# Kernel tuning notes

Hardware: AMD Instinct MI355X
Metric: run time of the kernel (lower is better)

## Reference

```python
import jax, jax.numpy as jnp
import numpy as np

N = 65536   # total nodes
E = 1048576 # total edges (avg degree 16)
B = 512     # graphs in batch
H = 4       # gat1 heads
C = 64      # per-head channels / GNN_HIDDEN


def segment_softmax(logits, seg, num_segments):
    # numerically stable softmax over segments (PyG softmax semantics, eps=1e-16)
    m = jax.ops.segment_max(logits, seg, num_segments=num_segments)
    m = jnp.where(jnp.isfinite(m), m, 0.0)
    e = jnp.exp(logits - m[seg])
    s = jax.ops.segment_sum(e, seg, num_segments=num_segments)
    return e / (s[seg] + 1e-16)


def gat_conv(x, edge_index, edge_attr, W, att_src, att_dst, We, att_edge, bias, heads, out_ch, concat):
    # PyG GATConv with edge_dim, add_self_loops=False
    n = x.shape[0]
    h = (x @ W).reshape(n, heads, out_ch)                 # (N,H,C)
    src, dst = edge_index[0], edge_index[1]
    a_s = jnp.sum(h * att_src, axis=-1)                   # (N,H)
    a_d = jnp.sum(h * att_dst, axis=-1)                   # (N,H)
    he = (edge_attr @ We).reshape(-1, heads, out_ch)      # (E,H,C)
    a_e = jnp.sum(he * att_edge, axis=-1)                 # (E,H)
    alpha = jax.nn.leaky_relu(a_s[src] + a_d[dst] + a_e, negative_slope=0.2)
    alpha = segment_softmax(alpha, dst, n)                # softmax over incoming edges per dst
    out = jax.ops.segment_sum(h[src] * alpha[..., None], dst, num_segments=n)  # (N,H,C)
    out = out.reshape(n, heads * out_ch) if concat else out.mean(axis=1)
    return out + bias


def setup_inputs() -> dict:
    key = jax.random.key(0)
    ks = jax.random.split(key, 24)
    s = 0.05
    d = {}
    d["global_feat"] = jax.random.normal(ks[0], (B, 512), jnp.float32)
    d["x"] = jax.random.normal(ks[1], (N, 13), jnp.float32)
    d["roi_feats"] = jax.random.normal(ks[2], (N, 256), jnp.float32)
    d["edge_index"] = jax.random.randint(ks[3], (2, E), 0, N)
    d["edge_attr"] = jax.random.normal(ks[4], (E, 5), jnp.float32)
    d["batch_vec"] = jnp.sort(jax.random.randint(ks[5], (N,), 0, B))
    # roi_proj / scene_proj
    d["roi_W"] = jax.random.normal(ks[6], (256, 64), jnp.float32) * s
    d["roi_b"] = jnp.zeros((64,), jnp.float32)
    d["scene_W"] = jax.random.normal(ks[7], (512, 128), jnp.float32) * s
    d["scene_b"] = jnp.zeros((128,), jnp.float32)
    d["g1_W"] = jax.random.normal(ks[8], (77, H * C), jnp.float32) * s
    d["g1_att_src"] = jax.random.normal(ks[9], (H, C), jnp.float32) * s
    d["g1_att_dst"] = jax.random.normal(ks[10], (H, C), jnp.float32) * s
    d["g1_We"] = jax.random.normal(ks[11], (5, H * C), jnp.float32) * s
    d["g1_att_edge"] = jax.random.normal(ks[12], (H, C), jnp.float32) * s
    d["g1_bias"] = jnp.zeros((H * C,), jnp.float32)
    # gat2: 256 -> 64, 1 head
    d["g2_W"] = jax.random.normal(ks[13], (H * C, C), jnp.float32) * s
    d["g2_att_src"] = jax.random.normal(ks[14], (1, C), jnp.float32) * s
    d["g2_att_dst"] = jax.random.normal(ks[15], (1, C), jnp.float32) * s
    d["g2_We"] = jax.random.normal(ks[16], (5, C), jnp.float32) * s
    d["g2_att_edge"] = jax.random.normal(ks[17], (1, C), jnp.float32) * s
    d["g2_bias"] = jnp.zeros((C,), jnp.float32)
    # attention pooling gate + classifier
    d["gate_W"] = jax.random.normal(ks[18], (C, 1), jnp.float32) * s
    d["gate_b"] = jnp.zeros((1,), jnp.float32)
    d["cls1_W"] = jax.random.normal(ks[19], (128 + C, 64), jnp.float32) * s
    d["cls1_b"] = jnp.zeros((64,), jnp.float32)
    d["cls2_W"] = jax.random.normal(ks[20], (64, 3), jnp.float32) * s
    d["cls2_b"] = jnp.zeros((3,), jnp.float32)
    return d


def reference(global_feat, x, roi_feats, edge_index, edge_attr, batch_vec,
              roi_W, roi_b, scene_W, scene_b,
              g1_W, g1_att_src, g1_att_dst, g1_We, g1_att_edge, g1_bias,
              g2_W, g2_att_src, g2_att_dst, g2_We, g2_att_edge, g2_bias,
              gate_W, gate_b, cls1_W, cls1_b, cls2_W, cls2_b):
    scene = global_feat @ scene_W + scene_b                       # (B,128)
    vis = jax.nn.relu(roi_feats @ roi_W + roi_b)                  # (N,64)
    h = jnp.concatenate([x, vis], axis=-1)                        # (N,77)
    h = jax.nn.relu(gat_conv(h, edge_index, edge_attr, g1_W, g1_att_src, g1_att_dst, g1_We, g1_att_edge, g1_bias, H, C, True))
    h = gat_conv(h, edge_index, edge_attr, g2_W, g2_att_src, g2_att_dst, g2_We, g2_att_edge, g2_bias, 1, C, False)  # (N,64)
    # GlobalAttention pooling
    gate = segment_softmax((h @ gate_W + gate_b)[:, 0], batch_vec, B)
    rel = jax.ops.segment_sum(gate[:, None] * h, batch_vec, num_segments=B)  # (B,64)
    comb = jnp.concatenate([scene, rel], axis=-1)                 # (B,192)
    hid = jax.nn.relu(comb @ cls1_W + cls1_b)                     # dropout off (eval)
    return hid @ cls2_W + cls2_b                                  # (B,3)
```

## Files before the change

kernel.cpp:

```cpp
#include <hip/hip_runtime.h>

#define N_NODES 65536
#define N_EDGES 1048576
#define NB      512

typedef unsigned short u16;
typedef unsigned int   u32;
typedef unsigned long long u64;

typedef __attribute__((ext_vector_type(8))) short bf16x8;
typedef __attribute__((ext_vector_type(4))) float f32x4;

__device__ __forceinline__ float bf2f(u16 u) { return __uint_as_float(((u32)u) << 16); }
__device__ __forceinline__ float lo16(u32 u) { return __uint_as_float(u << 16); }
__device__ __forceinline__ float hi16(u32 u) { return __uint_as_float(u & 0xffff0000u); }
__device__ __forceinline__ u16 f2bf(float f) {
    u32 u = __float_as_uint(f);
    u32 r = (u + 0x7fffu + ((u >> 16) & 1u)) >> 16;
    return (u16)r;
}
__device__ __forceinline__ u32 pk2(float a, float b) {
    return (u32)f2bf(a) | ((u32)f2bf(b) << 16);
}
__device__ __forceinline__ float wsum(float v) {
    for (int o = 32; o; o >>= 1) v += __shfl_xor(v, o, 64);
    return v;
}
__device__ __forceinline__ float wmax(float v) {
    for (int o = 32; o; o >>= 1) v = fmaxf(v, __shfl_xor(v, o, 64));
    return v;
}

__global__ void k_prep(const float* g1We, const float* g1ae, const float* g2We, const float* g2ae,
                       float* M1, float* M2) {
    int t = threadIdx.x;
    if (t < 20) {
        int j = t >> 2, h = t & 3;
        float s = 0.f;
        for (int c = 0; c < 64; c++) s += g1We[j * 256 + h * 64 + c] * g1ae[h * 64 + c];
        M1[t] = s;
    } else if (t < 25) {
        int j = t - 20;
        float s = 0.f;
        for (int c = 0; c < 64; c++) s += g2We[j * 64 + c] * g2ae[c];
        M2[j] = s;
    }
}

__global__ void k_wt1(const float* __restrict__ g1W, u16* __restrict__ Wt) {
    int c = blockIdx.x;
    int k = threadIdx.x;
    float v = 0.f;
    if (k < 77) {
        int ko = (k < 64) ? (13 + k) : (k - 64);
        v = g1W[(size_t)ko * 256 + c];
    }
    Wt[(size_t)c * 128 + k] = f2bf(v);
}

__global__ void k_prepv(const u16* __restrict__ Wt, const float* __restrict__ as_,
                        const float* __restrict__ ad_, float* __restrict__ v1s,
                        float* __restrict__ v1d) {
    int t = threadIdx.x;
    int h = t >> 7, k = t & 127;
    float s = 0.f, d = 0.f;
    for (int cc = 0; cc < 64; cc++) {
        float wv_ = bf2f(Wt[(size_t)(h * 64 + cc) * 128 + k]);
        s += wv_ * as_[h * 64 + cc];
        d += wv_ * ad_[h * 64 + cc];
    }
    v1s[t] = s;
    v1d[t] = d;
}

__global__ void k_wtv(const float* __restrict__ W, u16* __restrict__ Wt) {
    int c = blockIdx.x;
    int k = threadIdx.x;
    Wt[(size_t)c * 256 + k] = f2bf(W[(size_t)k * 64 + c]);
}

__global__ __launch_bounds__(256) void k_scene(const float* __restrict__ gf, const float* __restrict__ W,
                                               const float* __restrict__ bias, float* __restrict__ scene) {
    int idx = blockIdx.x * 256 + threadIdx.x;
    int b = idx >> 7, j = idx & 127;
    float acc = 0.f;
    for (int k = 0; k < 512; k++) acc += gf[b * 512 + k] * W[k * 128 + j];
    scene[idx] = acc + bias[j];
}

__global__ __launch_bounds__(256) void k_hist(const int* ei, int* cnt) {
    int e = blockIdx.x * 256 + threadIdx.x;
    atomicAdd(&cnt[ei[N_EDGES + e]], 1);
}

__global__ __launch_bounds__(256) void k_scan_blk(const int* __restrict__ cnt, int* __restrict__ pre,
                                                  int* __restrict__ bsum) {
    __shared__ int sd[256];
    int t = threadIdx.x, b = blockIdx.x;
    int base = b * 1024 + t * 4;
    int4 c = *(const int4*)(cnt + base);
    int s = c.x + c.y + c.z + c.w;
    sd[t] = s;
    __syncthreads();
    for (int off = 1; off < 256; off <<= 1) {
        int v = (t >= off) ? sd[t - off] : 0;
        __syncthreads();
        sd[t] += v;
        __syncthreads();
    }
    int excl = sd[t] - s;
    int4 p;
    p.x = excl;
    p.y = excl + c.x;
    p.z = excl + c.x + c.y;
    p.w = excl + c.x + c.y + c.z;
    *(int4*)(pre + base) = p;
    if (t == 255) bsum[b] = sd[255];
}

__global__ __launch_bounds__(64) void k_scan_top(int* bsum) {
    int t = threadIdx.x;
    int v = bsum[t];
    int inc = v;
    for (int off = 1; off < 64; off <<= 1) {
        int u = __shfl_up(inc, off, 64);
        if (t >= off) inc += u;
    }
    bsum[t] = inc - v;
}

__global__ __launch_bounds__(256) void k_scan_fix(const int* __restrict__ pre, const int* __restrict__ bsum,
                                                  int* __restrict__ row_ptr, int* __restrict__ coarse_cur) {
    int i = blockIdx.x * 256 + threadIdx.x;
    int v = pre[i] + bsum[i >> 10];
    row_ptr[i] = v;
    if ((i & 255) == 0) coarse_cur[i >> 8] = v;
    if (i == 0) row_ptr[N_NODES] = N_EDGES;
}

__global__ __launch_bounds__(256) void k_bucket(const int* __restrict__ ei, int* coarse_cur,
                                                u32* __restrict__ bpack, int* __restrict__ bsrc) {
    __shared__ u32 stageP[4096];
    __shared__ int stageS[4096];
    __shared__ int bcnt[256], bscan[256], boff[256], gbase[256];
    int t = threadIdx.x;
    int e0 = blockIdx.x * 4096;
    bcnt[t] = 0;
    __syncthreads();
    int dreg[16], sreg[16];
    for (int it = 0; it < 16; it++) {
        int e = e0 + it * 256 + t;
        int dd = ei[N_EDGES + e];
        dreg[it] = dd;
        sreg[it] = ei[e];
        atomicAdd(&bcnt[dd >> 8], 1);
    }
    __syncthreads();
    int v = bcnt[t];
    bscan[t] = v;
    __syncthreads();
    for (int off = 1; off < 256; off <<= 1) {
        int u = (t >= off) ? bscan[t - off] : 0;
        __syncthreads();
        bscan[t] += u;
        __syncthreads();
    }
    boff[t] = bscan[t] - v;
    gbase[t] = v ? atomicAdd(&coarse_cur[t], v) : 0;
    __syncthreads();
    for (int it = 0; it < 16; it++) {
        int e = e0 + it * 256 + t;
        int b = dreg[it] >> 8;
        int pos = atomicAdd(&boff[b], 1);
        stageP[pos] = ((u32)e << 12) | (u32)(dreg[it] & 255);
        stageS[pos] = sreg[it];
    }
    __syncthreads();
    for (int idx = t; idx < 4096; idx += 256) {
        int lo = 0, hi = 255;
        while (lo < hi) { int mid = (lo + hi) >> 1; if (bscan[mid] > idx) hi = mid; else lo = mid + 1; }
        int b = lo;
        int g = gbase[b] + (idx - (bscan[b] - bcnt[b]));
        bpack[g] = stageP[idx];
        bsrc[g] = stageS[idx];
    }
}

__global__ __launch_bounds__(256) void k_sortb(const u32* __restrict__ bpack, const int* __restrict__ bsrc,
                                               const int* __restrict__ row_ptr,
                                               int* __restrict__ eord, int* __restrict__ ssrc) {
    __shared__ int cur[256];
    int t = threadIdx.x, b = blockIdx.x;
    int nbase = b * 256;
    cur[t] = row_ptr[nbase + t];
    __syncthreads();
    int beg = row_ptr[nbase];
    int end = row_ptr[nbase + 256];
    for (int i = beg + t; i < end; i += 256) {
        u32 wd = bpack[i];
        int src = bsrc[i];
        int d8 = wd & 255;
        int pos = atomicAdd(&cur[d8], 1);
        eord[pos] = (int)(wd >> 12);
        ssrc[pos] = src;
    }
}

__global__ __launch_bounds__(256) void k_payload(const int* __restrict__ eord, const float* __restrict__ ea,
                                                 const float* __restrict__ M1, const float* __restrict__ M2,
                                                 float* __restrict__ a1es, float* __restrict__ a2es) {
    int pos = blockIdx.x * 256 + threadIdx.x;
    int e = eord[pos];
    float v[5];
    for (int j = 0; j < 5; j++) v[j] = ea[(size_t)e * 5 + j];
    float4 o;
    o.x = v[0]*M1[0]  + v[1]*M1[4]  + v[2]*M1[8]  + v[3]*M1[12] + v[4]*M1[16];
    o.y = v[0]*M1[1]  + v[1]*M1[5]  + v[2]*M1[9]  + v[3]*M1[13] + v[4]*M1[17];
    o.z = v[0]*M1[2]  + v[1]*M1[6]  + v[2]*M1[10] + v[3]*M1[14] + v[4]*M1[18];
    o.w = v[0]*M1[3]  + v[1]*M1[7]  + v[2]*M1[11] + v[3]*M1[15] + v[4]*M1[19];
    *(float4*)(a1es + (size_t)pos * 4) = o;
    a2es[pos] = v[0]*M2[0] + v[1]*M2[1] + v[2]*M2[2] + v[3]*M2[3] + v[4]*M2[4];
}

__global__ __launch_bounds__(256) void k_vis(const float* __restrict__ roi, const u16* __restrict__ Wt,
                                             const float* __restrict__ bias, const float* __restrict__ x,
                                             u16* __restrict__ featb) {
    __shared__ u16 At[64][264];
    int t = threadIdx.x;
    int w = t >> 6, l = t & 63, lo = l & 15, hi = l >> 4;
    int n0 = blockIdx.x * 64;
    int r = t >> 2, sub = t & 3;
    const float* rp = roi + (size_t)(n0 + r) * 256 + sub * 4;
    #pragma unroll
    for (int q = 0; q < 16; q++) {
        float4 v = *(const float4*)(rp + q * 16);
        uint2 p;
        p.x = pk2(v.x, v.y);
        p.y = pk2(v.z, v.w);
        *(uint2*)&At[r][q * 16 + sub * 4] = p;
    }
    {
        u16* fb = featb + (size_t)(n0 + r) * 128;
        if (sub == 0) {
            const float* xp = x + (size_t)(n0 + r) * 13;
            #pragma unroll
            for (int j = 0; j < 13; j++) fb[64 + j] = f2bf(xp[j]);
        } else {
            int j0 = 77 + (sub - 1) * 17;
            #pragma unroll
            for (int j = 0; j < 17; j++) fb[j0 + j] = 0;
        }
    }
    float bb[4][4];
    #pragma unroll
    for (int cb = 0; cb < 4; cb++)
        #pragma unroll
        for (int rg = 0; rg < 4; rg++) bb[cb][rg] = bias[cb * 16 + hi * 4 + rg];
    __syncthreads();
    f32x4 acc[4];
    #pragma unroll
    for (int cb = 0; cb < 4; cb++) acc[cb] = (f32x4){0.f, 0.f, 0.f, 0.f};
    #pragma unroll
    for (int ks = 0; ks < 8; ks++) {
        bf16x8 af = *(const bf16x8*)(&At[w * 16 + lo][ks * 32 + hi * 8]);
        #pragma unroll
        for (int cb = 0; cb < 4; cb++) {
            bf16x8 wf = *(const bf16x8*)(Wt + (size_t)(cb * 16 + lo) * 256 + ks * 32 + hi * 8);
            acc[cb] = __builtin_amdgcn_mfma_f32_16x16x32_bf16(wf, af, acc[cb], 0, 0, 0);
        }
    }
    int nrow = n0 + w * 16 + lo;
    #pragma unroll
    for (int cb = 0; cb < 4; cb++) {
        uint2 p;
        p.x = pk2(fmaxf(acc[cb][0] + bb[cb][0], 0.f), fmaxf(acc[cb][1] + bb[cb][1], 0.f));
        p.y = pk2(fmaxf(acc[cb][2] + bb[cb][2], 0.f), fmaxf(acc[cb][3] + bb[cb][3], 0.f));
        *(uint2*)(featb + (size_t)nrow * 128 + cb * 16 + hi * 4) = p;
    }
}

__global__ __launch_bounds__(256) void k_a1(const u16* __restrict__ featb, const float* __restrict__ v1s,
                                            const float* __restrict__ v1d,
                                            float* __restrict__ a1s, float* __restrict__ a1d) {
    __shared__ float vs[512], vd[512];
    int t = threadIdx.x;
    for (int idx = t; idx < 512; idx += 256) { vs[idx] = v1s[idx]; vd[idx] = v1d[idx]; }
    __syncthreads();
    int n = blockIdx.x * 32 + (t >> 3), l8 = t & 7;
    const uint4* fp = (const uint4*)(featb + (size_t)n * 128 + l8 * 16);
    uint4 u0 = fp[0], u1 = fp[1];
    float f[16];
    f[0]=lo16(u0.x); f[1]=hi16(u0.x); f[2]=lo16(u0.y); f[3]=hi16(u0.y);
    f[4]=lo16(u0.z); f[5]=hi16(u0.z); f[6]=lo16(u0.w); f[7]=hi16(u0.w);
    f[8]=lo16(u1.x); f[9]=hi16(u1.x); f[10]=lo16(u1.y); f[11]=hi16(u1.y);
    f[12]=lo16(u1.z); f[13]=hi16(u1.z); f[14]=lo16(u1.w); f[15]=hi16(u1.w);
    float as4[4], ad4[4];
    #pragma unroll
    for (int h = 0; h < 4; h++) {
        float s = 0.f, d = 0.f;
        #pragma unroll
        for (int q = 0; q < 4; q++) {
            float4 v4 = *(const float4*)&vs[h * 128 + l8 * 16 + q * 4];
            float4 w4 = *(const float4*)&vd[h * 128 + l8 * 16 + q * 4];
            s += f[q*4+0]*v4.x + f[q*4+1]*v4.y + f[q*4+2]*v4.z + f[q*4+3]*v4.w;
            d += f[q*4+0]*w4.x + f[q*4+1]*w4.y + f[q*4+2]*w4.z + f[q*4+3]*w4.w;
        }
        as4[h] = s; ad4[h] = d;
    }
    #pragma unroll
    for (int h = 0; h < 4; h++) {
        for (int o = 1; o < 8; o <<= 1) {
            as4[h] += __shfl_xor(as4[h], o, 64);
            ad4[h] += __shfl_xor(ad4[h], o, 64);
        }
    }
    if (l8 == 0) {
        *(float4*)(a1s + (size_t)n * 4) = make_float4(as4[0], as4[1], as4[2], as4[3]);
        *(float4*)(a1d + (size_t)n * 4) = make_float4(ad4[0], ad4[1], ad4[2], ad4[3]);
    }
}

__global__ __launch_bounds__(256) void k_sg1g(const int* __restrict__ row_ptr, const int* __restrict__ ssrc,
                                              const float* __restrict__ a1s, const float* __restrict__ a1d,
                                              const float* __restrict__ a1es, const u16* __restrict__ featb,
                                              u16* __restrict__ G) {
    __shared__ float wl[4][1024];
    int t = threadIdx.x;
    int wv = t >> 6, L = t & 63;
    int n = blockIdx.x * 4 + wv;
    int beg = row_ptr[n], deg = row_ptr[n + 1] - beg;
    int lim = (deg < 256) ? deg : 256;
    {
        int h = L >> 4, j = L & 15;
        float adn = a1d[n * 4 + h];
        float m = -3.0e38f, s = 0.f;
        for (int i = j; i < deg; i += 16) {
            int pos = beg + i;
            float l = a1s[ssrc[pos] * 4 + h] + adn + a1es[(size_t)pos * 4 + h];
            l = (l > 0.f) ? l : 0.2f * l;
            if (i < 256) wl[wv][i * 4 + h] = l;
            if (l > m) { s = s * __expf(m - l) + 1.f; m = l; }
            else       { s += __expf(l - m); }
        }
        for (int o = 1; o < 16; o <<= 1) {
            float mo = __shfl_xor(m, o, 64), so = __shfl_xor(s, o, 64);
            float M = fmaxf(m, mo);
            s = s * __expf(m - M) + so * __expf(mo - M);
            m = M;
        }
        float inv = 1.f / (s + 1e-16f);
        for (int i = j; i < lim; i += 16)
            wl[wv][i * 4 + h] = __expf(wl[wv][i * 4 + h] - m) * inv;
    }
    __syncthreads();
    int es = L >> 4;
    int cg = L & 15;
    float acc[4][8];
    #pragma unroll
    for (int h = 0; h < 4; h++)
        #pragma unroll
        for (int j2 = 0; j2 < 8; j2++) acc[h][j2] = 0.f;
    for (int i = 0; i < deg; i += 4) {
        int ii = i + es;
        bool v = ii < deg;
        int pos = v ? beg + ii : beg;
        int s = ssrc[pos];
        float4 al = v ? *(const float4*)&wl[wv][ii * 4] : make_float4(0.f, 0.f, 0.f, 0.f);
        uint4 u = *((const uint4*)(featb + (size_t)s * 128) + cg);
        float f0 = lo16(u.x), f1 = hi16(u.x), f2 = lo16(u.y), f3 = hi16(u.y);
        float f4 = lo16(u.z), f5 = hi16(u.z), f6 = lo16(u.w), f7 = hi16(u.w);
        #pragma unroll
        for (int h = 0; h < 4; h++) {
            float a = (&al.x)[h];
            acc[h][0] += a * f0; acc[h][1] += a * f1;
            acc[h][2] += a * f2; acc[h][3] += a * f3;
            acc[h][4] += a * f4; acc[h][5] += a * f5;
            acc[h][6] += a * f6; acc[h][7] += a * f7;
        }
    }
    #pragma unroll
    for (int h = 0; h < 4; h++)
        #pragma unroll
        for (int j2 = 0; j2 < 8; j2++) {
            acc[h][j2] += __shfl_xor(acc[h][j2], 16, 64);
            acc[h][j2] += __shfl_xor(acc[h][j2], 32, 64);
        }
    if (es == 0) {
        #pragma unroll
        for (int h = 0; h < 4; h++) {
            uint4 p;
            p.x = pk2(acc[h][0], acc[h][1]);
            p.y = pk2(acc[h][2], acc[h][3]);
            p.z = pk2(acc[h][4], acc[h][5]);
            p.w = pk2(acc[h][6], acc[h][7]);
            *((uint4*)(G + ((size_t)n * 4 + h) * 128) + cg) = p;
        }
    }
}

__global__ __launch_bounds__(256) void k_go1(const u16* __restrict__ G, const u16* __restrict__ Wt,
                                             const float* __restrict__ bias, u16* __restrict__ out1) {
    int t = threadIdx.x;
    int w = t >> 6, l = t & 63, lo = l & 15, hi = l >> 4;
    int n0 = blockIdx.x * 64;
    bf16x8 wf[4][4];
    float bb[4][4];
    #pragma unroll
    for (int cb = 0; cb < 4; cb++) {
        #pragma unroll
        for (int ks = 0; ks < 4; ks++)
            wf[cb][ks] = *(const bf16x8*)(Wt + (size_t)(w * 64 + cb * 16 + lo) * 128 + ks * 32 + hi * 8);
        #pragma unroll
        for (int rg = 0; rg < 4; rg++)
            bb[cb][rg] = bias[w * 64 + cb * 16 + hi * 4 + rg];
    }
    #pragma unroll
    for (int nb = 0; nb < 4; nb++) {
        f32x4 acc[4];
        #pragma unroll
        for (int cb = 0; cb < 4; cb++) acc[cb] = (f32x4){0.f, 0.f, 0.f, 0.f};
        int nrow = n0 + nb * 16 + lo;
        const u16* gp = G + ((size_t)nrow * 4 + w) * 128 + hi * 8;
        #pragma unroll
        for (int ks = 0; ks < 4; ks++) {
            bf16x8 af = *(const bf16x8*)(gp + ks * 32);
            #pragma unroll
            for (int cb = 0; cb < 4; cb++)
                acc[cb] = __builtin_amdgcn_mfma_f32_16x16x32_bf16(wf[cb][ks], af, acc[cb], 0, 0, 0);
        }
        #pragma unroll
        for (int cb = 0; cb < 4; cb++) {
            uint2 p;
            p.x = pk2(fmaxf(acc[cb][0] + bb[cb][0], 0.f), fmaxf(acc[cb][1] + bb[cb][1], 0.f));
            p.y = pk2(fmaxf(acc[cb][2] + bb[cb][2], 0.f), fmaxf(acc[cb][3] + bb[cb][3], 0.f));
            *(uint2*)(out1 + (size_t)nrow * 256 + w * 64 + cb * 16 + hi * 4) = p;
        }
    }
}

__global__ __launch_bounds__(256) void k_h2(const u16* __restrict__ A, const u16* __restrict__ Wt,
                                            const float* __restrict__ as_, const float* __restrict__ ad_,
                                            u16* __restrict__ out, float* __restrict__ a2s,
                                            float* __restrict__ a2d) {
    int t = threadIdx.x;
    int w = t >> 6, l = t & 63, lo = l & 15, hi = l >> 4;
    int nrow = blockIdx.x * 64 + w * 16 + lo;
    f32x4 acc[4];
    #pragma unroll
    for (int cb = 0; cb < 4; cb++) acc[cb] = (f32x4){0.f, 0.f, 0.f, 0.f};
    const u16* ap = A + (size_t)nrow * 256 + hi * 8;
    #pragma unroll
    for (int ks = 0; ks < 8; ks++) {
        bf16x8 af = *(const bf16x8*)(ap + ks * 32);
        #pragma unroll
        for (int cb = 0; cb < 4; cb++) {
            bf16x8 wf = *(const bf16x8*)(Wt + (size_t)(cb * 16 + lo) * 256 + ks * 32 + hi * 8);
            acc[cb] = __builtin_amdgcn_mfma_f32_16x16x32_bf16(wf, af, acc[cb], 0, 0, 0);
        }
    }
    float ps = 0.f, pd = 0.f;
    #pragma unroll
    for (int cb = 0; cb < 4; cb++) {
        uint2 p;
        p.x = pk2(acc[cb][0], acc[cb][1]);
        p.y = pk2(acc[cb][2], acc[cb][3]);
        *(uint2*)(out + (size_t)nrow * 64 + cb * 16 + hi * 4) = p;
        #pragma unroll
        for (int rg = 0; rg < 4; rg++) {
            float a = acc[cb][rg];
            ps += a * as_[cb * 16 + hi * 4 + rg];
            pd += a * ad_[cb * 16 + hi * 4 + rg];
        }
    }
    ps += __shfl_xor(ps, 16, 64); ps += __shfl_xor(ps, 32, 64);
    pd += __shfl_xor(pd, 16, 64); pd += __shfl_xor(pd, 32, 64);
    if (hi == 0) {
        a2s[nrow] = ps;
        a2d[nrow] = pd;
    }
}

__global__ __launch_bounds__(256) void k_sg2(const int* __restrict__ row_ptr, const int* __restrict__ ssrc,
                                             const float* __restrict__ a2s, const float* __restrict__ a2d,
                                             const float* __restrict__ a2es, const u16* __restrict__ h2b,
                                             const float* __restrict__ bias, float* __restrict__ hfin) {
    __shared__ float wl[4][256];
    int t = threadIdx.x;
    int wv = t >> 6, L = t & 63;
    int n = blockIdx.x * 4 + wv;
    int beg = row_ptr[n], deg = row_ptr[n + 1] - beg;
    int lim = (deg < 256) ? deg : 256;
    {
        float adn = a2d[n];
        float m = -3.0e38f, s = 0.f;
        for (int i = L; i < deg; i += 64) {
            int pos = beg + i;
            float l = a2s[ssrc[pos]] + adn + a2es[pos];
            l = (l > 0.f) ? l : 0.2f * l;
            if (i < 256) wl[wv][i] = l;
            if (l > m) { s = s * __expf(m - l) + 1.f; m = l; }
            else       { s += __expf(l - m); }
        }
        for (int o = 1; o < 64; o <<= 1) {
            float mo = __shfl_xor(m, o, 64), so = __shfl_xor(s, o, 64);
            float M = fmaxf(m, mo);
            s = s * __expf(m - M) + so * __expf(mo - M);
            m = M;
        }
        float inv = 1.f / (s + 1e-16f);
        for (int i = L; i < lim; i += 64)
            wl[wv][i] = __expf(wl[wv][i] - m) * inv;
    }
    __syncthreads();
    int halfE = L >> 5;
    int L32 = L & 31;
    float a0 = 0.f, a1v = 0.f;
    int last = beg + deg - 1;
    const u32* h2u = (const u32*)h2b;
    for (int i = 0; i < deg; i += 8) {
        int iA = i + halfE, iB = i + 2 + halfE, iC = i + 4 + halfE, iD = i + 6 + halfE;
        bool vA = iA < deg, vB = iB < deg, vC = iC < deg, vD = iD < deg;
        int cA = vA ? beg + iA : last, cB = vB ? beg + iB : last;
        int cC = vC ? beg + iC : last, cD = vD ? beg + iD : last;
        int sA = ssrc[cA], sB = ssrc[cB], sC = ssrc[cC], sD = ssrc[cD];
        float wA = vA ? wl[wv][iA] : 0.f;
        float wB = vB ? wl[wv][iB] : 0.f;
        float wC = vC ? wl[wv][iC] : 0.f;
        float wD = vD ? wl[wv][iD] : 0.f;
        u32 uA = h2u[(size_t)sA * 32 + L32];
        u32 uB = h2u[(size_t)sB * 32 + L32];
        u32 uC = h2u[(size_t)sC * 32 + L32];
        u32 uD = h2u[(size_t)sD * 32 + L32];
        a0  += wA * lo16(uA) + wB * lo16(uB) + wC * lo16(uC) + wD * lo16(uD);
        a1v += wA * hi16(uA) + wB * hi16(uB) + wC * hi16(uC) + wD * hi16(uD);
    }
    a0  += __shfl_xor(a0, 32, 64);
    a1v += __shfl_xor(a1v, 32, 64);
    if (halfE == 0) {
        float2 o;
        o.x = a0  + bias[2 * L32];
        o.y = a1v + bias[2 * L32 + 1];
        *(float2*)(hfin + (size_t)n * 64 + 2 * L32) = o;
    }
}

__global__ __launch_bounds__(64) void k_pool(const int* __restrict__ bvec, const float* __restrict__ hf,
                                             const float* gateW, const float* gateb,
                                             const float* __restrict__ scene,
                                             const float* c1W, const float* c1b,
                                             const float* c2W, const float* c2b,
                                             float* __restrict__ outp) {
    int b = blockIdx.x, lane = threadIdx.x;
    __shared__ float gwl[64], se[64], comb[192], hid[64];
    gwl[lane] = gateW[lane];
    __syncthreads();
    int s0, s1;
    { int lo = 0, hi = N_NODES; while (lo < hi) { int mid = (lo + hi) >> 1; if (bvec[mid] < b) lo = mid + 1; else hi = mid; } s0 = lo; }
    { int lo = 0, hi = N_NODES; while (lo < hi) { int mid = (lo + hi) >> 1; if (bvec[mid] < b + 1) lo = mid + 1; else hi = mid; } s1 = lo; }
    float gb = gateb[0];
    float m = -3.0e38f, ssum = 0.f, acc = 0.f;
    for (int cs = s0; cs < s1; cs += 64) {
        int cnt = min(64, s1 - cs);
        float l = -3.0e38f;
        if (lane < cnt) {
            int n = cs + lane;
            float d = 0.f;
            for (int i = 0; i < 64; i++) d += hf[(size_t)n * 64 + i] * gwl[i];
            l = d + gb;
        }
        float cm = wmax(l);
        float newm = fmaxf(m, cm);
        float rsc = __expf(m - newm);
        float e = (lane < cnt) ? __expf(l - newm) : 0.f;
        float es = wsum(e);
        ssum = ssum * rsc + es;
        se[lane] = e;
        __syncthreads();
        float a2 = 0.f;
        for (int i = 0; i < cnt; i++) a2 += se[i] * hf[(size_t)(cs + i) * 64 + lane];
        acc = acc * rsc + a2;
        __syncthreads();
        m = newm;
    }
    float rel = acc / (ssum + 1e-16f);
    comb[lane] = scene[b * 128 + lane];
    comb[64 + lane] = scene[b * 128 + 64 + lane];
    comb[128 + lane] = rel;
    __syncthreads();
    float hj = 0.f;
    for (int k = 0; k < 192; k++) hj += comb[k] * c1W[k * 64 + lane];
    hj += c1b[lane];
    hid[lane] = fmaxf(hj, 0.f);
    __syncthreads();
    if (lane < 3) {
        float o = 0.f;
        for (int k = 0; k < 64; k++) o += hid[k] * c2W[k * 3 + lane];
        o += c2b[lane];
        outp[b * 3 + lane] = o;
    }
}

extern "C" void kernel_launch(void* const* d_in, const int* in_sizes, int n_in,
                              void* d_out, int out_size, void* d_ws, size_t ws_size,
                              hipStream_t stream) {
    (void)in_sizes; (void)n_in; (void)out_size; (void)ws_size;
    const float* gf     = (const float*)d_in[0];
    const float* x      = (const float*)d_in[1];
    const float* roi    = (const float*)d_in[2];
    const int*   ei     = (const int*)d_in[3];
    const float* ea     = (const float*)d_in[4];
    const int*   bvec   = (const int*)d_in[5];
    const float* roiW   = (const float*)d_in[6];
    const float* roib   = (const float*)d_in[7];
    const float* sceneW = (const float*)d_in[8];
    const float* sceneb = (const float*)d_in[9];
    const float* g1W    = (const float*)d_in[10];
    const float* g1as   = (const float*)d_in[11];
    const float* g1ad   = (const float*)d_in[12];
    const float* g1We   = (const float*)d_in[13];
    const float* g1ae   = (const float*)d_in[14];
    const float* g1b    = (const float*)d_in[15];
    const float* g2W    = (const float*)d_in[16];
    const float* g2as   = (const float*)d_in[17];
    const float* g2ad   = (const float*)d_in[18];
    const float* g2We   = (const float*)d_in[19];
    const float* g2ae   = (const float*)d_in[20];
    const float* g2b    = (const float*)d_in[21];
    const float* gateW  = (const float*)d_in[22];
    const float* gateb  = (const float*)d_in[23];
    const float* c1W    = (const float*)d_in[24];
    const float* c1b    = (const float*)d_in[25];
    const float* c2W    = (const float*)d_in[26];
    const float* c2b    = (const float*)d_in[27];

    char* w = (char*)d_ws;
    size_t o = 0;
    auto nxt = [&](size_t bytes) -> char* {
        char* p = w + o;
        o += (bytes + 255) & ~(size_t)255;
        return p;
    };
    float* scene  = (float*)nxt((size_t)NB * 128 * 4);
    float* M1     = (float*)nxt(80);
    float* M2     = (float*)nxt(32);
    u16* g1Wt     = (u16*)nxt((size_t)256 * 128 * 2);
    u16* roiWt    = (u16*)nxt((size_t)64 * 256 * 2);
    u16* g2Wt     = (u16*)nxt((size_t)64 * 256 * 2);
    float* v1s    = (float*)nxt(512 * 4);
    float* v1d    = (float*)nxt(512 * 4);
    int* cnt      = (int*)nxt((size_t)N_NODES * 4);
    int* pre      = (int*)nxt((size_t)N_NODES * 4);
    int* bsum     = (int*)nxt(64 * 4);
    int* row_ptr  = (int*)nxt((size_t)(N_NODES + 1) * 4);
    int* coarse   = (int*)nxt(256 * 4);
    u32* bpack    = (u32*)nxt((size_t)N_EDGES * 4);
    int* bsrc     = (int*)nxt((size_t)N_EDGES * 4);
    int* eord     = (int*)nxt((size_t)N_EDGES * 4);
    int* ssrc     = (int*)nxt((size_t)N_EDGES * 4);
    float* a1es   = (float*)nxt((size_t)N_EDGES * 16);
    float* a2es   = (float*)nxt((size_t)N_EDGES * 4);
    u16* featb    = (u16*)nxt((size_t)N_NODES * 128 * 2);
    u16* G        = (u16*)nxt((size_t)N_NODES * 4 * 128 * 2);
    u16* out1     = (u16*)nxt((size_t)N_NODES * 256 * 2);
    u16* h2b      = (u16*)nxt((size_t)N_NODES * 64 * 2);
    float* hfin   = (float*)nxt((size_t)N_NODES * 64 * 4);
    float* a1s    = (float*)nxt((size_t)N_NODES * 16);
    float* a1d    = (float*)nxt((size_t)N_NODES * 16);
    float* a2s    = (float*)nxt((size_t)N_NODES * 4);
    float* a2d    = (float*)nxt((size_t)N_NODES * 4);

    hipMemsetAsync(cnt, 0, (size_t)N_NODES * 4, stream);
    k_prep<<<1, 32, 0, stream>>>(g1We, g1ae, g2We, g2ae, M1, M2);
    k_wt1<<<256, 128, 0, stream>>>(g1W, g1Wt);
    k_prepv<<<1, 512, 0, stream>>>(g1Wt, g1as, g1ad, v1s, v1d);
    k_wtv<<<64, 256, 0, stream>>>(roiW, roiWt);
    k_wtv<<<64, 256, 0, stream>>>(g2W, g2Wt);
    k_scene<<<(NB * 128) / 256, 256, 0, stream>>>(gf, sceneW, sceneb, scene);
    k_hist<<<N_EDGES / 256, 256, 0, stream>>>(ei, cnt);
    k_scan_blk<<<64, 256, 0, stream>>>(cnt, pre, bsum);
    k_scan_top<<<1, 64, 0, stream>>>(bsum);
    k_scan_fix<<<N_NODES / 256, 256, 0, stream>>>(pre, bsum, row_ptr, coarse);
    k_bucket<<<256, 256, 0, stream>>>(ei, coarse, bpack, bsrc);
    k_sortb<<<256, 256, 0, stream>>>(bpack, bsrc, row_ptr, eord, ssrc);
    k_payload<<<N_EDGES / 256, 256, 0, stream>>>(eord, ea, M1, M2, a1es, a2es);
    k_vis<<<N_NODES / 64, 256, 0, stream>>>(roi, roiWt, roib, x, featb);
    k_a1<<<N_NODES / 32, 256, 0, stream>>>(featb, v1s, v1d, a1s, a1d);
    k_sg1g<<<N_NODES / 4, 256, 0, stream>>>(row_ptr, ssrc, a1s, a1d, a1es, featb, G);
    k_go1<<<N_NODES / 64, 256, 0, stream>>>(G, g1Wt, g1b, out1);
    k_h2<<<N_NODES / 64, 256, 0, stream>>>(out1, g2Wt, g2as, g2ad, h2b, a2s, a2d);
    k_sg2<<<N_NODES / 4, 256, 0, stream>>>(row_ptr, ssrc, a2s, a2d, a2es, h2b, g2b, hfin);
    k_pool<<<NB, 64, 0, stream>>>(bvec, hfin, gateW, gateb, scene, c1W, c1b, c2W, c2b, (float*)d_out);
}
```

Measured before the change: 550.9 us.

## Fuse weight prep, sort+payload, and GAT1 output+GAT2 projection kernels; prefetch in gather

Merges five small weight-preparation kernels into one launch and folds the edge payload computation into the per-bucket sort kernel, which drops the eord buffer and one pass over edges. Fuses the GAT1 output GEMM with the GAT2 projection through swizzled LDS, so the 32 MB out1 intermediate never goes to global memory. In the first gather kernel, source indices are cached in LDS, the block barrier becomes a wave-local waitcnt, and the next neighbor's features are prefetched one step ahead. The cost is more register and LDS pressure, and the wave-local sync depends on each wave touching only its own LDS slice.

Result: no change. 544.0 us (-1.2%).

```diff
diff --git a/kernel.cpp b/kernel.cpp
--- a/kernel.cpp
+++ b/kernel.cpp
@@ -31,52 +31,56 @@
     return v;
 }
 
-__global__ void k_prep(const float* g1We, const float* g1ae, const float* g2We, const float* g2ae,
-                       float* M1, float* M2) {
-    int t = threadIdx.x;
-    if (t < 20) {
-        int j = t >> 2, h = t & 3;
-        float s = 0.f;
-        for (int c = 0; c < 64; c++) s += g1We[j * 256 + h * 64 + c] * g1ae[h * 64 + c];
-        M1[t] = s;
-    } else if (t < 25) {
-        int j = t - 20;
-        float s = 0.f;
-        for (int c = 0; c < 64; c++) s += g2We[j * 64 + c] * g2ae[c];
-        M2[j] = s;
-    }
-}
-
-__global__ void k_wt1(const float* __restrict__ g1W, u16* __restrict__ Wt) {
-    int c = blockIdx.x;
-    int k = threadIdx.x;
-    float v = 0.f;
-    if (k < 77) {
-        int ko = (k < 64) ? (13 + k) : (k - 64);
-        v = g1W[(size_t)ko * 256 + c];
-    }
-    Wt[(size_t)c * 128 + k] = f2bf(v);
-}
-
-__global__ void k_prepv(const u16* __restrict__ Wt, const float* __restrict__ as_,
-                        const float* __restrict__ ad_, float* __restrict__ v1s,
-                        float* __restrict__ v1d) {
-    int t = threadIdx.x;
-    int h = t >> 7, k = t & 127;
-    float s = 0.f, d = 0.f;
-    for (int cc = 0; cc < 64; cc++) {
-        float wv_ = bf2f(Wt[(size_t)(h * 64 + cc) * 128 + k]);
-        s += wv_ * as_[h * 64 + cc];
-        d += wv_ * ad_[h * 64 + cc];
-    }
-    v1s[t] = s;
-    v1d[t] = d;
-}
-
-__global__ void k_wtv(const float* __restrict__ W, u16* __restrict__ Wt) {
-    int c = blockIdx.x;
-    int k = threadIdx.x;
-    Wt[(size_t)c * 256 + k] = f2bf(W[(size_t)k * 64 + c]);
+__global__ __launch_bounds__(512) void k_wprep(const float* __restrict__ g1W, const float* __restrict__ roiW,
+                                               const float* __restrict__ g2W,
+                                               const float* __restrict__ g1as, const float* __restrict__ g1ad,
+                                               const float* __restrict__ g1We, const float* __restrict__ g1ae,
+                                               const float* __restrict__ g2We, const float* __restrict__ g2ae,
+                                               u16* __restrict__ g1Wt, u16* __restrict__ roiWt,
+                                               u16* __restrict__ g2Wt, float* __restrict__ v1s,
+                                               float* __restrict__ v1d, float* __restrict__ M1,
+                                               float* __restrict__ M2) {
+    int b = blockIdx.x, t = threadIdx.x;
+    if (b < 64) {
+        int c = b * 4 + (t >> 7), k = t & 127;
+        float v = 0.f;
+        if (k < 77) {
+            int ko = (k < 64) ? (13 + k) : (k - 64);
+            v = g1W[(size_t)ko * 256 + c];
+        }
+        g1Wt[(size_t)c * 128 + k] = f2bf(v);
+    } else if (b < 96) {
+        int c = (b - 64) * 2 + (t >> 8), k = t & 255;
+        roiWt[(size_t)c * 256 + k] = f2bf(roiW[(size_t)k * 64 + c]);
+    } else if (b < 128) {
+        int c = (b - 96) * 2 + (t >> 8), k = t & 255;
+        g2Wt[(size_t)c * 256 + k] = f2bf(g2W[(size_t)k * 64 + c]);
+    } else if (b == 128) {
+        int h = t >> 7, k = t & 127;
+        float s = 0.f, d = 0.f;
+        if (k < 77) {
+            int ko = (k < 64) ? (13 + k) : (k - 64);
+            for (int cc = 0; cc < 64; cc++) {
+                float wv_ = g1W[(size_t)ko * 256 + h * 64 + cc];
+                s += wv_ * g1as[h * 64 + cc];
+                d += wv_ * g1ad[h * 64 + cc];
+            }
+        }
+        v1s[t] = s;
+        v1d[t] = d;
+    } else {
+        if (t < 20) {
+            int j = t >> 2, h = t & 3;
+            float s = 0.f;
+            for (int c = 0; c < 64; c++) s += g1We[j * 256 + h * 64 + c] * g1ae[h * 64 + c];
+            M1[t] = s;
+        } else if (t < 25) {
+            int j = t - 20;
+            float s = 0.f;
+            for (int c = 0; c < 64; c++) s += g2We[j * 64 + c] * g2ae[c];
+            M2[j] = s;
+        }
+    }
 }
 
 __global__ __launch_bounds__(256) void k_scene(const float* __restrict__ gf, const float* __restrict__ W,
@@ -186,40 +190,40 @@
     }
 }
 
-__global__ __launch_bounds__(256) void k_sortb(const u32* __restrict__ bpack, const int* __restrict__ bsrc,
-                                               const int* __restrict__ row_ptr,
-                                               int* __restrict__ eord, int* __restrict__ ssrc) {
+__global__ __launch_bounds__(256) void k_sortp(const u32* __restrict__ bpack, const int* __restrict__ bsrc,
+                                               const int* __restrict__ row_ptr, const float* __restrict__ ea,
+                                               const float* __restrict__ M1, const float* __restrict__ M2,
+                                               int* __restrict__ ssrc, float* __restrict__ a1es,
+                                               float* __restrict__ a2es) {
     __shared__ int cur[256];
     int t = threadIdx.x, b = blockIdx.x;
     int nbase = b * 256;
     cur[t] = row_ptr[nbase + t];
     __syncthreads();
+    float m1[20], m2[5];
+    #pragma unroll
+    for (int j = 0; j < 20; j++) m1[j] = M1[j];
+    #pragma unroll
+    for (int j = 0; j < 5; j++) m2[j] = M2[j];
     int beg = row_ptr[nbase];
     int end = row_ptr[nbase + 256];
     for (int i = beg + t; i < end; i += 256) {
         u32 wd = bpack[i];
         int src = bsrc[i];
         int d8 = wd & 255;
+        int e = (int)(wd >> 12);
         int pos = atomicAdd(&cur[d8], 1);
-        eord[pos] = (int)(wd >> 12);
         ssrc[pos] = src;
-    }
-}
-
-__global__ __launch_bounds__(256) void k_payload(const int* __restrict__ eord, const float* __restrict__ ea,
-                                                 const float* __restrict__ M1, const float* __restrict__ M2,
-                                                 float* __restrict__ a1es, float* __restrict__ a2es) {
-    int pos = blockIdx.x * 256 + threadIdx.x;
-    int e = eord[pos];
-    float v[5];
-    for (int j = 0; j < 5; j++) v[j] = ea[(size_t)e * 5 + j];
-    float4 o;
-    o.x = v[0]*M1[0]  + v[1]*M1[4]  + v[2]*M1[8]  + v[3]*M1[12] + v[4]*M1[16];
-    o.y = v[0]*M1[1]  + v[1]*M1[5]  + v[2]*M1[9]  + v[3]*M1[13] + v[4]*M1[17];
-    o.z = v[0]*M1[2]  + v[1]*M1[6]  + v[2]*M1[10] + v[3]*M1[14] + v[4]*M1[18];
-    o.w = v[0]*M1[3]  + v[1]*M1[7]  + v[2]*M1[11] + v[3]*M1[15] + v[4]*M1[19];
-    *(float4*)(a1es + (size_t)pos * 4) = o;
-    a2es[pos] = v[0]*M2[0] + v[1]*M2[1] + v[2]*M2[2] + v[3]*M2[3] + v[4]*M2[4];
+        const float* ep = ea + (size_t)e * 5;
+        float v0 = ep[0], v1 = ep[1], v2 = ep[2], v3 = ep[3], v4 = ep[4];
+        float4 o;
+        o.x = v0*m1[0]  + v1*m1[4]  + v2*m1[8]  + v3*m1[12] + v4*m1[16];
+        o.y = v0*m1[1]  + v1*m1[5]  + v2*m1[9]  + v3*m1[13] + v4*m1[17];
+        o.z = v0*m1[2]  + v1*m1[6]  + v2*m1[10] + v3*m1[14] + v4*m1[18];
+        o.w = v0*m1[3]  + v1*m1[7]  + v2*m1[11] + v3*m1[15] + v4*m1[19];
+        *(float4*)(a1es + (size_t)pos * 4) = o;
+        a2es[pos] = v0*m2[0] + v1*m2[1] + v2*m2[2] + v3*m2[3] + v4*m2[4];
+    }
 }
 
 __global__ __launch_bounds__(256) void k_vis(const float* __restrict__ roi, const u16* __restrict__ Wt,
@@ -325,6 +329,7 @@
                                               const float* __restrict__ a1es, const u16* __restrict__ featb,
                                               u16* __restrict__ G) {
     __shared__ float wl[4][1024];
+    __shared__ int   sl[4][256];
     int t = threadIdx.x;
     int wv = t >> 6, L = t & 63;
     int n = blockIdx.x * 4 + wv;
@@ -336,7 +341,9 @@
         float m = -3.0e38f, s = 0.f;
         for (int i = j; i < deg; i += 16) {
             int pos = beg + i;
-            float l = a1s[ssrc[pos] * 4 + h] + adn + a1es[(size_t)pos * 4 + h];
+            int sv = ssrc[pos];
+            if (h == 0 && i < 256) sl[wv][i] = sv;
+            float l = a1s[sv * 4 + h] + adn + a1es[(size_t)pos * 4 + h];
             l = (l > 0.f) ? l : 0.2f * l;
             if (i < 256) wl[wv][i * 4 + h] = l;
             if (l > m) { s = s * __expf(m - l) + 1.f; m = l; }
@@ -352,7 +359,8 @@
         for (int i = j; i < lim; i += 16)
             wl[wv][i * 4 + h] = __expf(wl[wv][i * 4 + h] - m) * inv;
     }
-    __syncthreads();
+    asm volatile("" ::: "memory");
+    __builtin_amdgcn_s_waitcnt(0);
     int es = L >> 4;
     int cg = L & 15;
     float acc[4][8];
@@ -360,23 +368,28 @@
     for (int h = 0; h < 4; h++)
         #pragma unroll
         for (int j2 = 0; j2 < 8; j2++) acc[h][j2] = 0.f;
+    int ii0 = es;
+    bool v0 = ii0 < deg;
+    int s0 = v0 ? sl[wv][ii0] : 0;
+    float4 al0 = v0 ? *(const float4*)&wl[wv][ii0 * 4] : make_float4(0.f, 0.f, 0.f, 0.f);
+    uint4 u0 = *((const uint4*)(featb + (size_t)s0 * 128) + cg);
     for (int i = 0; i < deg; i += 4) {
-        int ii = i + es;
-        bool v = ii < deg;
-        int pos = v ? beg + ii : beg;
-        int s = ssrc[pos];
-        float4 al = v ? *(const float4*)&wl[wv][ii * 4] : make_float4(0.f, 0.f, 0.f, 0.f);
-        uint4 u = *((const uint4*)(featb + (size_t)s * 128) + cg);
-        float f0 = lo16(u.x), f1 = hi16(u.x), f2 = lo16(u.y), f3 = hi16(u.y);
-        float f4 = lo16(u.z), f5 = hi16(u.z), f6 = lo16(u.w), f7 = hi16(u.w);
+        int iin = i + 4 + es;
+        bool vn = iin < deg;
+        int sn = vn ? sl[wv][iin] : 0;
+        float4 aln = vn ? *(const float4*)&wl[wv][iin * 4] : make_float4(0.f, 0.f, 0.f, 0.f);
+        uint4 un = *((const uint4*)(featb + (size_t)sn * 128) + cg);
+        float f0 = lo16(u0.x), f1 = hi16(u0.x), f2 = lo16(u0.y), f3 = hi16(u0.y);
+        float f4 = lo16(u0.z), f5 = hi16(u0.z), f6 = lo16(u0.w), f7 = hi16(u0.w);
         #pragma unroll
         for (int h = 0; h < 4; h++) {
-            float a = (&al.x)[h];
+            float a = (&al0.x)[h];
             acc[h][0] += a * f0; acc[h][1] += a * f1;
             acc[h][2] += a * f2; acc[h][3] += a * f3;
             acc[h][4] += a * f4; acc[h][5] += a * f5;
             acc[h][6] += a * f6; acc[h][7] += a * f7;
         }
+        u0 = un; al0 = aln;
     }
     #pragma unroll
     for (int h = 0; h < 4; h++)
@@ -398,76 +411,69 @@
     }
 }
 
-__global__ __launch_bounds__(256) void k_go1(const u16* __restrict__ G, const u16* __restrict__ Wt,
-                                             const float* __restrict__ bias, u16* __restrict__ out1) {
-    int t = threadIdx.x;
-    int w = t >> 6, l = t & 63, lo = l & 15, hi = l >> 4;
-    int n0 = blockIdx.x * 64;
-    bf16x8 wf[4][4];
-    float bb[4][4];
-    #pragma unroll
-    for (int cb = 0; cb < 4; cb++) {
-        #pragma unroll
-        for (int ks = 0; ks < 4; ks++)
-            wf[cb][ks] = *(const bf16x8*)(Wt + (size_t)(w * 64 + cb * 16 + lo) * 128 + ks * 32 + hi * 8);
-        #pragma unroll
-        for (int rg = 0; rg < 4; rg++)
-            bb[cb][rg] = bias[w * 64 + cb * 16 + hi * 4 + rg];
-    }
-    #pragma unroll
-    for (int nb = 0; nb < 4; nb++) {
-        f32x4 acc[4];
-        #pragma unroll
-        for (int cb = 0; cb < 4; cb++) acc[cb] = (f32x4){0.f, 0.f, 0.f, 0.f};
-        int nrow = n0 + nb * 16 + lo;
-        const u16* gp = G + ((size_t)nrow * 4 + w) * 128 + hi * 8;
-        #pragma unroll
-        for (int ks = 0; ks < 4; ks++) {
-            bf16x8 af = *(const bf16x8*)(gp + ks * 32);
-            #pragma unroll
-            for (int cb = 0; cb < 4; cb++)
-                acc[cb] = __builtin_amdgcn_mfma_f32_16x16x32_bf16(wf[cb][ks], af, acc[cb], 0, 0, 0);
-        }
-        #pragma unroll
-        for (int cb = 0; cb < 4; cb++) {
-            uint2 p;
-            p.x = pk2(fmaxf(acc[cb][0] + bb[cb][0], 0.f), fmaxf(acc[cb][1] + bb[cb][1], 0.f));
-            p.y = pk2(fmaxf(acc[cb][2] + bb[cb][2], 0.f), fmaxf(acc[cb][3] + bb[cb][3], 0.f));
-            *(uint2*)(out1 + (size_t)nrow * 256 + w * 64 + cb * 16 + hi * 4) = p;
-        }
-    }
-}
-
-__global__ __launch_bounds__(256) void k_h2(const u16* __restrict__ A, const u16* __restrict__ Wt,
-                                            const float* __restrict__ as_, const float* __restrict__ ad_,
-                                            u16* __restrict__ out, float* __restrict__ a2s,
-                                            float* __restrict__ a2d) {
+__global__ __launch_bounds__(256) void k_goh(const u16* __restrict__ G, const u16* __restrict__ Wt1,
+                                             const float* __restrict__ b1, const u16* __restrict__ Wt2,
+                                             const float* __restrict__ as_, const float* __restrict__ ad_,
+                                             u16* __restrict__ h2b, float* __restrict__ a2s,
+                                             float* __restrict__ a2d) {
+    __shared__ u16 T[4][4096];
     int t = threadIdx.x;
     int w = t >> 6, l = t & 63, lo = l & 15, hi = l >> 4;
     int nrow = blockIdx.x * 64 + w * 16 + lo;
-    f32x4 acc[4];
-    #pragma unroll
-    for (int cb = 0; cb < 4; cb++) acc[cb] = (f32x4){0.f, 0.f, 0.f, 0.f};
-    const u16* ap = A + (size_t)nrow * 256 + hi * 8;
+    char* Tw = (char*)&T[w][0];
+    #pragma unroll
+    for (int h = 0; h < 4; h++) {
+        const u16* gp = G + ((size_t)nrow * 4 + h) * 128 + hi * 8;
+        bf16x8 af0 = *(const bf16x8*)(gp);
+        bf16x8 af1 = *(const bf16x8*)(gp + 32);
+        bf16x8 af2 = *(const bf16x8*)(gp + 64);
+        bf16x8 af3 = *(const bf16x8*)(gp + 96);
+        f32x4 acc[4];
+        #pragma unroll
+        for (int cb = 0; cb < 4; cb++) acc[cb] = (f32x4){0.f, 0.f, 0.f, 0.f};
+        #pragma unroll
+        for (int cb = 0; cb < 4; cb++) {
+            const u16* wp = Wt1 + (size_t)(h * 64 + cb * 16 + lo) * 128 + hi * 8;
+            acc[cb] = __builtin_amdgcn_mfma_f32_16x16x32_bf16(*(const bf16x8*)(wp),       af0, acc[cb], 0, 0, 0);
+            acc[cb] = __builtin_amdgcn_mfma_f32_16x16x32_bf16(*(const bf16x8*)(wp + 32),  af1, acc[cb], 0, 0, 0);
+            acc[cb] = __builtin_amdgcn_mfma_f32_16x16x32_bf16(*(const bf16x8*)(wp + 64),  af2, acc[cb], 0, 0, 0);
+            acc[cb] = __builtin_amdgcn_mfma_f32_16x16x32_bf16(*(const bf16x8*)(wp + 96),  af3, acc[cb], 0, 0, 0);
+        }
+        #pragma unroll
+        for (int cb = 0; cb < 4; cb++) {
+            int ch0 = h * 64 + cb * 16 + hi * 4;
+            float4 bb = *(const float4*)(b1 + ch0);
+            uint2 p;
+            p.x = pk2(fmaxf(acc[cb][0] + bb.x, 0.f), fmaxf(acc[cb][1] + bb.y, 0.f));
+            p.y = pk2(fmaxf(acc[cb][2] + bb.z, 0.f), fmaxf(acc[cb][3] + bb.w, 0.f));
+            u32 byte = (u32)(lo * 512 + ch0 * 2) ^ ((u32)(lo & 7) << 4);
+            *(uint2*)(Tw + byte) = p;
+        }
+    }
+    __syncthreads();
+    f32x4 acc2[4];
+    #pragma unroll
+    for (int cb = 0; cb < 4; cb++) acc2[cb] = (f32x4){0.f, 0.f, 0.f, 0.f};
     #pragma unroll
     for (int ks = 0; ks < 8; ks++) {
-        bf16x8 af = *(const bf16x8*)(ap + ks * 32);
+        u32 byte = (u32)(lo * 512 + (ks * 32 + hi * 8) * 2) ^ ((u32)(lo & 7) << 4);
+        bf16x8 bf = *(const bf16x8*)(Tw + byte);
         #pragma unroll
         for (int cb = 0; cb < 4; cb++) {
-            bf16x8 wf = *(const bf16x8*)(Wt + (size_t)(cb * 16 + lo) * 256 + ks * 32 + hi * 8);
-            acc[cb] = __builtin_amdgcn_mfma_f32_16x16x32_bf16(wf, af, acc[cb], 0, 0, 0);
+            bf16x8 wf = *(const bf16x8*)(Wt2 + (size_t)(cb * 16 + lo) * 256 + ks * 32 + hi * 8);
+            acc2[cb] = __builtin_amdgcn_mfma_f32_16x16x32_bf16(wf, bf, acc2[cb], 0, 0, 0);
         }
     }
     float ps = 0.f, pd = 0.f;
     #pragma unroll
     for (int cb = 0; cb < 4; cb++) {
         uint2 p;
-        p.x = pk2(acc[cb][0], acc[cb][1]);
-        p.y = pk2(acc[cb][2], acc[cb][3]);
-        *(uint2*)(out + (size_t)nrow * 64 + cb * 16 + hi * 4) = p;
+        p.x = pk2(acc2[cb][0], acc2[cb][1]);
+        p.y = pk2(acc2[cb][2], acc2[cb][3]);
+        *(uint2*)(h2b + (size_t)nrow * 64 + cb * 16 + hi * 4) = p;
         #pragma unroll
         for (int rg = 0; rg < 4; rg++) {
-            float a = acc[cb][rg];
+            float a = acc2[cb][rg];
             ps += a * as_[cb * 16 + hi * 4 + rg];
             pd += a * ad_[cb * 16 + hi * 4 + rg];
         }
@@ -655,13 +661,11 @@
     int* coarse   = (int*)nxt(256 * 4);
     u32* bpack    = (u32*)nxt((size_t)N_EDGES * 4);
     int* bsrc     = (int*)nxt((size_t)N_EDGES * 4);
-    int* eord     = (int*)nxt((size_t)N_EDGES * 4);
     int* ssrc     = (int*)nxt((size_t)N_EDGES * 4);
     float* a1es   = (float*)nxt((size_t)N_EDGES * 16);
     float* a2es   = (float*)nxt((size_t)N_EDGES * 4);
     u16* featb    = (u16*)nxt((size_t)N_NODES * 128 * 2);
     u16* G        = (u16*)nxt((size_t)N_NODES * 4 * 128 * 2);
-    u16* out1     = (u16*)nxt((size_t)N_NODES * 256 * 2);
     u16* h2b      = (u16*)nxt((size_t)N_NODES * 64 * 2);
     float* hfin   = (float*)nxt((size_t)N_NODES * 64 * 4);
     float* a1s    = (float*)nxt((size_t)N_NODES * 16);
@@ -670,24 +674,19 @@
     float* a2d    = (float*)nxt((size_t)N_NODES * 4);
 
     hipMemsetAsync(cnt, 0, (size_t)N_NODES * 4, stream);
-    k_prep<<<1, 32, 0, stream>>>(g1We, g1ae, g2We, g2ae, M1, M2);
-    k_wt1<<<256, 128, 0, stream>>>(g1W, g1Wt);
-    k_prepv<<<1, 512, 0, stream>>>(g1Wt, g1as, g1ad, v1s, v1d);
-    k_wtv<<<64, 256, 0, stream>>>(roiW, roiWt);
-    k_wtv<<<64, 256, 0, stream>>>(g2W, g2Wt);
+    k_wprep<<<130, 512, 0, stream>>>(g1W, roiW, g2W, g1as, g1ad, g1We, g1ae, g2We, g2ae,
+                                     g1Wt, roiWt, g2Wt, v1s, v1d, M1, M2);
     k_scene<<<(NB * 128) / 256, 256, 0, stream>>>(gf, sceneW, sceneb, scene);
     k_hist<<<N_EDGES / 256, 256, 0, stream>>>(ei, cnt);
     k_scan_blk<<<64, 256, 0, stream>>>(cnt, pre, bsum);
     k_scan_top<<<1, 64, 0, stream>>>(bsum);
     k_scan_fix<<<N_NODES / 256, 256, 0, stream>>>(pre, bsum, row_ptr, coarse);
     k_bucket<<<256, 256, 0, stream>>>(ei, coarse, bpack, bsrc);
-    k_sortb<<<256, 256, 0, stream>>>(bpack, bsrc, row_ptr, eord, ssrc);
-    k_payload<<<N_EDGES / 256, 256, 0, stream>>>(eord, ea, M1, M2, a1es, a2es);
+    k_sortp<<<256, 256, 0, stream>>>(bpack, bsrc, row_ptr, ea, M1, M2, ssrc, a1es, a2es);
     k_vis<<<N_NODES / 64, 256, 0, stream>>>(roi, roiWt, roib, x, featb);
     k_a1<<<N_NODES / 32, 256, 0, stream>>>(featb, v1s, v1d, a1s, a1d);
     k_sg1g<<<N_NODES / 4, 256, 0, stream>>>(row_ptr, ssrc, a1s, a1d, a1es, featb, G);
-    k_go1<<<N_NODES / 64, 256, 0, stream>>>(G, g1Wt, g1b, out1);
-    k_h2<<<N_NODES / 64, 256, 0, stream>>>(out1, g2Wt, g2as, g2ad, h2b, a2s, a2d);
+    k_goh<<<N_NODES / 64, 256, 0, stream>>>(G, g1Wt, g1b, g2Wt, g2as, g2ad, h2b, a2s, a2d);
     k_sg2<<<N_NODES / 4, 256, 0, stream>>>(row_ptr, ssrc, a2s, a2d, a2es, h2b, g2b, hfin);
     k_pool<<<NB, 64, 0, stream>>>(bvec, hfin, gateW, gateb, scene, c1W, c1b, c2W, c2b, (float*)d_out);
 }
```
